# Optimization experiments

Hardware: AMD Instinct MI355X
Metric: run time of the kernel (lower is better)

## Reference

```python
import jax, jax.numpy as jnp
import numpy as np

TEMPERATURE = 0.5
N, D = 8192, 256
N_CLASSES = 64


def setup_inputs() -> dict:
    key = jax.random.key(0)
    k1, k2 = jax.random.split(key)
    emb = jax.random.normal(k1, (N, D), dtype=jnp.float32)
    # original module expects normalized embeddings
    emb = emb / jnp.linalg.norm(emb, axis=-1, keepdims=True)
    labels = jax.random.randint(k2, (N,), 0, N_CLASSES, dtype=jnp.int64)
    return {"embeddings": emb, "epitope_labels": labels}


def reference(embeddings, epitope_labels):
    n = embeddings.shape[0]
    # [N, N] pairwise similarities
    sim = jnp.matmul(embeddings, embeddings.T) / TEMPERATURE
    eye = jnp.eye(n, dtype=bool)
    labels_eq = epitope_labels[None, :] == epitope_labels[:, None]
    mask_pos = labels_eq & ~eye  # positives exclude self
    # row-max subtraction (detached, matches torch .detach())
    sim_max = jax.lax.stop_gradient(jnp.max(sim, axis=1, keepdims=True))
    shifted = sim - sim_max
    exp_sim = jnp.exp(shifted)
    # denominator excludes the diagonal (self-similarity)
    denom = jnp.sum(jnp.where(eye, 0.0, exp_sim), axis=1)  # [N]
    # per-pair loss: -log(exp_sim_ij / denom_i) = -(shifted_ij - log denom_i)
    per_pair = -(shifted - jnp.log(denom)[:, None])
    # mean over positive pairs (equivalent to masked_select + repeat_interleave + mean)
    n_pos = jnp.sum(mask_pos)
    loss = jnp.sum(jnp.where(mask_pos, per_pair, 0.0)) / n_pos
    return loss
```

## Files before the change

### kernel.cpp

```cpp
#include <hip/hip_runtime.h>
#include <hip/hip_bf16.h>

#define N 8192
#define D 256
#define NC 64

typedef __attribute__((ext_vector_type(8))) short bf16x8;
typedef __attribute__((ext_vector_type(4))) float f32x4;

#define BM 256
#define CT 64
#define NTILE 8
#define GRID 512

#define K1 2.8853900817779268f
#define K2 (-2.8853900817779268f)

__device__ inline unsigned short f2bf(float x) {
    __hip_bfloat16 h = __float2bfloat16(x);
    return *reinterpret_cast<unsigned short*>(&h);
}

__device__ inline float fast_exp2(float t) {
#if __has_builtin(__builtin_amdgcn_exp2f)
    return __builtin_amdgcn_exp2f(t);
#else
    return __expf(t * 0.69314718056f);
#endif
}

__global__ void convert_kernel(const float4* __restrict__ E4, ushort4* __restrict__ Ebf4,
                               float* __restrict__ Z, float* __restrict__ S) {
    int i = blockIdx.x * blockDim.x + threadIdx.x;
    if (i < (N * D) / 4) {
        float4 v = E4[i];
        ushort4 o;
        o.x = f2bf(v.x); o.y = f2bf(v.y); o.z = f2bf(v.z); o.w = f2bf(v.w);
        Ebf4[i] = o;
    }
    if (i < N) Z[i] = 0.0f;
    if (i < NC * D) S[i] = 0.0f;
}

__global__ __launch_bounds__(256)
void classsum_kernel(const float* __restrict__ emb, const int* __restrict__ labels,
                     float* __restrict__ S) {
    __shared__ float Sl[NC * D];
    int t = threadIdx.x;
    for (int i = t; i < NC * D; i += 256) Sl[i] = 0.0f;
    __syncthreads();
    int rbase = blockIdx.x * 64;
    for (int r = 0; r < 64; ++r) {
        int i = rbase + r;
        int lab = labels[i];
        Sl[lab * D + t] += emb[(size_t)i * D + t];
    }
    __syncthreads();
    for (int i = t; i < NC * D; i += 256) atomicAdd(&S[i], Sl[i]);
}

__global__ __launch_bounds__(256, 2)
void sim_kernel(const __hip_bfloat16* __restrict__ Ebf, float* __restrict__ Z) {
    __shared__ unsigned char Bsh[2 * 32768];

    const int tid  = threadIdx.x;
    const int lane = tid & 63;
    const int w    = tid >> 6;
    const int r0   = (blockIdx.x >> 4) * BM;
    const int c0   = (blockIdx.x & 15) * (CT * NTILE);
    const char* eb = (const char*)Ebf;

    bf16x8 a[4][8];
#pragma unroll
    for (int rg = 0; rg < 4; ++rg) {
        int row = r0 + w * 64 + rg * 16 + (lane & 15);
        const char* rp = eb + (size_t)row * 512 + ((lane >> 4) * 16);
#pragma unroll
        for (int kg = 0; kg < 8; ++kg)
            a[rg][kg] = *reinterpret_cast<const bf16x8*>(rp + kg * 64);
    }

    float zacc[4][4];
#pragma unroll
    for (int rg = 0; rg < 4; ++rg)
#pragma unroll
        for (int r = 0; r < 4; ++r) zacc[rg][r] = 0.0f;

    const int seg = (lane & 3) ^ ((lane >> 3) & 3);
    const char* sbase = eb + (size_t)(c0 + (lane >> 2)) * 512 + seg * 16;

    const unsigned rb0 =
        (unsigned)((lane & 15) * 64 +
                   (((lane >> 4) ^ (((lane & 15) >> 1) & 3)) << 4));

    auto stage = [&](int buf, int t) {
#pragma unroll
        for (int m = 0; m < 8; ++m) {
            int c = w * 8 + m;
            int kg = c >> 2, colblk = c & 3;
            __builtin_amdgcn_global_load_lds(
                (const __attribute__((address_space(1))) void*)
                    (sbase + (size_t)t * (CT * 512) + colblk * 8192 + kg * 64),
                (__attribute__((address_space(3))) void*)
                    (Bsh + buf * 32768 + kg * 4096 + colblk * 1024),
                16, 0, 0);
        }
    };

    auto do_tile = [&](int t, int buf) {
        if (t + 1 < NTILE) stage(buf ^ 1, t + 1);

        f32x4 acc[4][4];
#pragma unroll
        for (int rg = 0; rg < 4; ++rg)
#pragma unroll
            for (int cg = 0; cg < 4; ++cg) acc[rg][cg] = (f32x4){0.f, 0.f, 0.f, 0.f};

#pragma unroll
        for (int kg = 0; kg < 8; ++kg) {
            bf16x8 b[4];
#pragma unroll
            for (int cg = 0; cg < 4; ++cg)
                b[cg] = *reinterpret_cast<const bf16x8*>(
                    Bsh + buf * 32768 + kg * 4096 + cg * 1024 + rb0);
#pragma unroll
            for (int rg = 0; rg < 4; ++rg)
#pragma unroll
                for (int cg = 0; cg < 4; ++cg)
                    acc[rg][cg] = __builtin_amdgcn_mfma_f32_16x16x32_bf16(
                        a[rg][kg], b[cg], acc[rg][cg], 0, 0, 0);
        }

#pragma unroll
        for (int rg = 0; rg < 4; ++rg)
#pragma unroll
            for (int r = 0; r < 4; ++r) {
                float s = zacc[rg][r];
#pragma unroll
                for (int cg = 0; cg < 4; ++cg)
                    s += fast_exp2(__builtin_fmaf(acc[rg][cg][r], K1, K2));
                zacc[rg][r] = s;
            }

        __syncthreads();
    };

    stage(0, 0);
    __syncthreads();
    for (int t = 0; t < NTILE; t += 2) {
        do_tile(t, 0);
        do_tile(t + 1, 1);
    }

#pragma unroll
    for (int rg = 0; rg < 4; ++rg)
#pragma unroll
        for (int r = 0; r < 4; ++r) {
            float z = zacc[rg][r];
#pragma unroll
            for (int m = 1; m <= 8; m <<= 1) z += __shfl_xor(z, m, 64);
            if ((lane & 15) == 0) {
                int row = r0 + w * 64 + rg * 16 + (lane >> 4) * 4 + r;
                atomicAdd(&Z[row], z);
            }
        }
}

__global__ __launch_bounds__(1024)
void finalize_kernel(const float* __restrict__ Z, const float* __restrict__ S,
                     const int* __restrict__ labels, float* __restrict__ out) {
    __shared__ int hist[NC];
    __shared__ float s0[1024], s1[1024];
    int t = threadIdx.x;
    if (t < NC) hist[t] = 0;
    __syncthreads();
    for (int i = t; i < N; i += 1024) atomicAdd(&hist[labels[i]], 1);
    __syncthreads();

    float num = 0.0f, den = 0.0f;
    for (int i = t; i < N; i += 1024) {
        float z = Z[i] - 1.0f;
        float c = (float)(hist[labels[i]] - 1);
        num += c * (2.0f + __logf(z));
        den += c;
    }
    float ss = 0.0f;
    for (int i = t; i < NC * D; i += 1024) { float v = S[i]; ss += v * v; }
    num -= 2.0f * ss / 1.0f;

    s0[t] = num; s1[t] = den;
    __syncthreads();
    for (int s = 512; s > 0; s >>= 1) {
        if (t < s) { s0[t] += s0[t + s]; s1[t] += s1[t + s]; }
        __syncthreads();
    }
    if (t == 0) out[0] = (s0[0] + 2.0f * (float)N) / s1[0];
}

extern "C" void kernel_launch(void* const* d_in, const int* in_sizes, int n_in,
                              void* d_out, int out_size, void* d_ws, size_t ws_size,
                              hipStream_t stream) {
    const float* emb  = (const float*)d_in[0];
    const int* labels = (const int*)d_in[1];
    float* out = (float*)d_out;

    char* ws = (char*)d_ws;
    __hip_bfloat16* Ebf = (__hip_bfloat16*)ws;
    float* Z = (float*)(ws + (size_t)N * D * 2);
    float* S = Z + N;

    convert_kernel<<<(N * D / 4 + 255) / 256, 256, 0, stream>>>(
        (const float4*)emb, (ushort4*)Ebf, Z, S);
    classsum_kernel<<<N / 64, 256, 0, stream>>>(emb, labels, S);
    sim_kernel<<<GRID, 256, 0, stream>>>(Ebf, Z);
    finalize_kernel<<<1, 1024, 0, stream>>>(Z, S, labels, out);
}
```

Before: 123.6 us.

## Fuse positive-pair sums into sim kernel with 256x256 tiles and 4-stage K pipeline

Drops the class-sum kernel. Positive-pair similarities are now accumulated per row directly from the MFMA results using label comparisons, which removes the 64x256 class-sum reduction and its atomics. The sim kernel moves from A-in-registers with column tiles to 256x256 output tiles per 512-thread block, with both operands staged in LDS across a 4-buffer pipeline over K (chunks of 32) and MFMA priority raised. Each block now computes a single exp pass over its tile. The costs are 128KB of LDS per block with launch_bounds(512,2), heavier register pressure from 32 accumulators per wave, and a positive-pair sum that now comes from bf16 products rather than fp32 class sums.

```diff
diff --git a/kernel.cpp b/kernel.cpp
--- a/kernel.cpp
+++ b/kernel.cpp
@@ -7,11 +7,6 @@
 
 typedef __attribute__((ext_vector_type(8))) short bf16x8;
 typedef __attribute__((ext_vector_type(4))) float f32x4;
-
-#define BM 256
-#define CT 64
-#define NTILE 8
-#define GRID 512
 
 #define K1 2.8853900817779268f
 #define K2 (-2.8853900817779268f)
@@ -30,7 +25,7 @@
 }
 
 __global__ void convert_kernel(const float4* __restrict__ E4, ushort4* __restrict__ Ebf4,
-                               float* __restrict__ Z, float* __restrict__ S) {
+                               float* __restrict__ Z, float* __restrict__ P) {
     int i = blockIdx.x * blockDim.x + threadIdx.x;
     if (i < (N * D) / 4) {
         float4 v = E4[i];
@@ -38,136 +33,121 @@
         o.x = f2bf(v.x); o.y = f2bf(v.y); o.z = f2bf(v.z); o.w = f2bf(v.w);
         Ebf4[i] = o;
     }
-    if (i < N) Z[i] = 0.0f;
-    if (i < NC * D) S[i] = 0.0f;
+    if (i < N) { Z[i] = 0.0f; P[i] = 0.0f; }
 }
 
-__global__ __launch_bounds__(256)
-void classsum_kernel(const float* __restrict__ emb, const int* __restrict__ labels,
-                     float* __restrict__ S) {
-    __shared__ float Sl[NC * D];
-    int t = threadIdx.x;
-    for (int i = t; i < NC * D; i += 256) Sl[i] = 0.0f;
-    __syncthreads();
-    int rbase = blockIdx.x * 64;
-    for (int r = 0; r < 64; ++r) {
-        int i = rbase + r;
-        int lab = labels[i];
-        Sl[lab * D + t] += emb[(size_t)i * D + t];
-    }
-    __syncthreads();
-    for (int i = t; i < NC * D; i += 256) atomicAdd(&S[i], Sl[i]);
-}
-
-__global__ __launch_bounds__(256, 2)
-void sim_kernel(const __hip_bfloat16* __restrict__ Ebf, float* __restrict__ Z) {
-    __shared__ unsigned char Bsh[2 * 32768];
+__global__ __launch_bounds__(512, 2)
+void sim_kernel(const __hip_bfloat16* __restrict__ Ebf,
+                const int* __restrict__ labels,
+                float* __restrict__ Z, float* __restrict__ P) {
+    __shared__ unsigned char Bsh[4 * 32768];
 
     const int tid  = threadIdx.x;
     const int lane = tid & 63;
-    const int w    = tid >> 6;
-    const int r0   = (blockIdx.x >> 4) * BM;
-    const int c0   = (blockIdx.x & 15) * (CT * NTILE);
+    const int wid  = tid >> 6;
+    const int wrow = wid >> 2;
+    const int wcol = wid & 3;
+    const int l15  = lane & 15;
+    const int l4   = lane >> 4;
+    const int p    = blockIdx.x >> 5;
+    const int q    = blockIdx.x & 31;
     const char* eb = (const char*)Ebf;
 
-    bf16x8 a[4][8];
+    auto stage = [&](int g) {
+        const unsigned bufb = (unsigned)(g & 3) * 32768u;
+        const char* kbase = eb + (size_t)g * 64;
 #pragma unroll
-    for (int rg = 0; rg < 4; ++rg) {
-        int row = r0 + w * 64 + rg * 16 + (lane & 15);
-        const char* rp = eb + (size_t)row * 512 + ((lane >> 4) * 16);
-#pragma unroll
-        for (int kg = 0; kg < 8; ++kg)
-            a[rg][kg] = *reinterpret_cast<const bf16x8*>(rp + kg * 64);
-    }
-
-    float zacc[4][4];
-#pragma unroll
-    for (int rg = 0; rg < 4; ++rg)
-#pragma unroll
-        for (int r = 0; r < 4; ++r) zacc[rg][r] = 0.0f;
-
-    const int seg = (lane & 3) ^ ((lane >> 3) & 3);
-    const char* sbase = eb + (size_t)(c0 + (lane >> 2)) * 512 + seg * 16;
-
-    const unsigned rb0 =
-        (unsigned)((lane & 15) * 64 +
-                   (((lane >> 4) ^ (((lane & 15) >> 1) & 3)) << 4));
-
-    auto stage = [&](int buf, int t) {
-#pragma unroll
-        for (int m = 0; m < 8; ++m) {
-            int c = w * 8 + m;
-            int kg = c >> 2, colblk = c & 3;
+        for (int j = 0; j < 4; ++j) {
+            int slot = (j & 1) * 512 + wid * 64 + lane;
+            int rc   = slot >> 2;
+            int s    = slot & 3;
+            int ss   = s ^ ((rc >> 1) & 3);
+            int base = (j >= 2) ? (q * 256) : (p * 256);
+            unsigned dest = bufb + ((j >= 2) ? 16384u : 0u) + (unsigned)slot * 16u;
+            const char* src = kbase + (size_t)(base + rc) * 512 + ss * 16;
             __builtin_amdgcn_global_load_lds(
-                (const __attribute__((address_space(1))) void*)
-                    (sbase + (size_t)t * (CT * 512) + colblk * 8192 + kg * 64),
-                (__attribute__((address_space(3))) void*)
-                    (Bsh + buf * 32768 + kg * 4096 + colblk * 1024),
-                16, 0, 0);
+                (const __attribute__((address_space(1))) void*)src,
+                (__attribute__((address_space(3))) void*)(Bsh + dest), 16, 0, 0);
         }
     };
 
-    auto do_tile = [&](int t, int buf) {
-        if (t + 1 < NTILE) stage(buf ^ 1, t + 1);
+    stage(0);
+    stage(1);
 
-        f32x4 acc[4][4];
+    int labP[8], labj[4];
 #pragma unroll
-        for (int rg = 0; rg < 4; ++rg)
+    for (int rg = 0; rg < 8; ++rg) {
+        int rr = p * 256 + wrow * 128 + rg * 16 + l4 * 4;
+        labP[rg] = labels[rr] | (labels[rr + 1] << 8) |
+                   (labels[rr + 2] << 16) | (labels[rr + 3] << 24);
+    }
 #pragma unroll
-            for (int cg = 0; cg < 4; ++cg) acc[rg][cg] = (f32x4){0.f, 0.f, 0.f, 0.f};
+    for (int cg = 0; cg < 4; ++cg)
+        labj[cg] = labels[q * 256 + wcol * 64 + cg * 16 + l15];
 
+    const unsigned laneOff = (unsigned)(l15 * 64 + ((l4 ^ ((l15 >> 1) & 3)) << 4));
+
+    f32x4 acc[8][4];
 #pragma unroll
-        for (int kg = 0; kg < 8; ++kg) {
-            bf16x8 b[4];
+    for (int rg = 0; rg < 8; ++rg)
+#pragma unroll
+        for (int cg = 0; cg < 4; ++cg) acc[rg][cg] = (f32x4){0.f, 0.f, 0.f, 0.f};
+
+    for (int g = 0; g < 8; ++g) {
+        if (g < 7) { asm volatile("s_waitcnt vmcnt(4)" ::: "memory"); }
+        else       { asm volatile("s_waitcnt vmcnt(0)" ::: "memory"); }
+        __builtin_amdgcn_s_barrier();
+        if (g + 2 < 8) stage(g + 2);
+
+        const unsigned bufb = (unsigned)(g & 3) * 32768u;
+        const unsigned ab = bufb + (unsigned)wrow * 8192u + laneOff;
+        const unsigned bb = bufb + 16384u + (unsigned)wcol * 4096u + laneOff;
+
+        bf16x8 af[8], bf[4];
+#pragma unroll
+        for (int rg = 0; rg < 8; ++rg)
+            af[rg] = *reinterpret_cast<const bf16x8*>(Bsh + ab + rg * 1024);
+#pragma unroll
+        for (int cg = 0; cg < 4; ++cg)
+            bf[cg] = *reinterpret_cast<const bf16x8*>(Bsh + bb + cg * 1024);
+
+        __builtin_amdgcn_s_setprio(1);
+#pragma unroll
+        for (int rg = 0; rg < 8; ++rg)
 #pragma unroll
             for (int cg = 0; cg < 4; ++cg)
-                b[cg] = *reinterpret_cast<const bf16x8*>(
-                    Bsh + buf * 32768 + kg * 4096 + cg * 1024 + rb0);
-#pragma unroll
-            for (int rg = 0; rg < 4; ++rg)
-#pragma unroll
-                for (int cg = 0; cg < 4; ++cg)
-                    acc[rg][cg] = __builtin_amdgcn_mfma_f32_16x16x32_bf16(
-                        a[rg][kg], b[cg], acc[rg][cg], 0, 0, 0);
-        }
-
-#pragma unroll
-        for (int rg = 0; rg < 4; ++rg)
-#pragma unroll
-            for (int r = 0; r < 4; ++r) {
-                float s = zacc[rg][r];
-#pragma unroll
-                for (int cg = 0; cg < 4; ++cg)
-                    s += fast_exp2(__builtin_fmaf(acc[rg][cg][r], K1, K2));
-                zacc[rg][r] = s;
-            }
-
-        __syncthreads();
-    };
-
-    stage(0, 0);
-    __syncthreads();
-    for (int t = 0; t < NTILE; t += 2) {
-        do_tile(t, 0);
-        do_tile(t + 1, 1);
+                acc[rg][cg] = __builtin_amdgcn_mfma_f32_16x16x32_bf16(
+                    af[rg], bf[cg], acc[rg][cg], 0, 0, 0);
+        __builtin_amdgcn_s_setprio(0);
     }
 
 #pragma unroll
-    for (int rg = 0; rg < 4; ++rg)
+    for (int rg = 0; rg < 8; ++rg)
 #pragma unroll
         for (int r = 0; r < 4; ++r) {
-            float z = zacc[rg][r];
+            int li = (labP[rg] >> (r * 8)) & 255;
+            float z = 0.0f, pp = 0.0f;
 #pragma unroll
-            for (int m = 1; m <= 8; m <<= 1) z += __shfl_xor(z, m, 64);
-            if ((lane & 15) == 0) {
-                int row = r0 + w * 64 + rg * 16 + (lane >> 4) * 4 + r;
+            for (int cg = 0; cg < 4; ++cg) {
+                float dd = acc[rg][cg][r];
+                z  += fast_exp2(__builtin_fmaf(dd, K1, K2));
+                pp += (li == labj[cg]) ? dd : 0.0f;
+            }
+#pragma unroll
+            for (int m = 1; m <= 8; m <<= 1) {
+                z  += __shfl_xor(z, m, 64);
+                pp += __shfl_xor(pp, m, 64);
+            }
+            if (l15 == 0) {
+                int row = p * 256 + wrow * 128 + rg * 16 + l4 * 4 + r;
                 atomicAdd(&Z[row], z);
+                atomicAdd(&P[row], pp);
             }
         }
 }
 
 __global__ __launch_bounds__(1024)
-void finalize_kernel(const float* __restrict__ Z, const float* __restrict__ S,
+void finalize_kernel(const float* __restrict__ Z, const float* __restrict__ P,
                      const int* __restrict__ labels, float* __restrict__ out) {
     __shared__ int hist[NC];
     __shared__ float s0[1024], s1[1024];
@@ -180,21 +160,18 @@
     float num = 0.0f, den = 0.0f;
     for (int i = t; i < N; i += 1024) {
         float z = Z[i] - 1.0f;
+        float pv = 2.0f * (P[i] - 1.0f);
         float c = (float)(hist[labels[i]] - 1);
-        num += c * (2.0f + __logf(z));
+        num += c * (2.0f + __logf(z)) - pv;
         den += c;
     }
-    float ss = 0.0f;
-    for (int i = t; i < NC * D; i += 1024) { float v = S[i]; ss += v * v; }
-    num -= 2.0f * ss / 1.0f;
-
     s0[t] = num; s1[t] = den;
     __syncthreads();
     for (int s = 512; s > 0; s >>= 1) {
         if (t < s) { s0[t] += s0[t + s]; s1[t] += s1[t + s]; }
         __syncthreads();
     }
-    if (t == 0) out[0] = (s0[0] + 2.0f * (float)N) / s1[0];
+    if (t == 0) out[0] = s0[0] / s1[0];
 }
 
 extern "C" void kernel_launch(void* const* d_in, const int* in_sizes, int n_in,
@@ -207,11 +184,10 @@
     char* ws = (char*)d_ws;
     __hip_bfloat16* Ebf = (__hip_bfloat16*)ws;
     float* Z = (float*)(ws + (size_t)N * D * 2);
-    float* S = Z + N;
+    float* P = Z + N;
 
     convert_kernel<<<(N * D / 4 + 255) / 256, 256, 0, stream>>>(
-        (const float4*)emb, (ushort4*)Ebf, Z, S);
-    classsum_kernel<<<N / 64, 256, 0, stream>>>(emb, labels, S);
-    sim_kernel<<<GRID, 256, 0, stream>>>(Ebf, Z);
-    finalize_kernel<<<1, 1024, 0, stream>>>(Z, S, labels, out);
+        (const float4*)emb, (ushort4*)Ebf, Z, P);
+    sim_kernel<<<1024, 512, 0, stream>>>(Ebf, labels, Z, P);
+    finalize_kernel<<<1, 1024, 0, stream>>>(Z, P, labels, out);
 }
```

Result: slower. 192.0 us (+55.3%).
